# Kernel optimization log

Hardware: AMD Instinct MI355X
Metric: run time of the kernel (lower is better)

## Reference

```python
import jax, jax.numpy as jnp
import numpy as np

N_HEADS = 8
HEAD_D = 64


def setup_inputs() -> dict:
    key = jax.random.key(0)
    ks = jax.random.split(key, 7)
    b, ds, dc = 4, 4096, 256
    ls, lc = 512, 512
    inner = N_HEADS * HEAD_D  # 512
    out_dim = 512
    data = jax.random.normal(ks[0], (b, ds, dc), dtype=jnp.float32)
    latent = jax.random.normal(ks[1], (b, ls, lc), dtype=jnp.float32)
    # torch nn.Linear weights are [out_features, in_features]
    Wq = jax.random.normal(ks[2], (inner, lc), dtype=jnp.float32) * (lc ** -0.5)
    Wk = jax.random.normal(ks[3], (inner, dc), dtype=jnp.float32) * (dc ** -0.5)
    Wv = jax.random.normal(ks[4], (inner, dc), dtype=jnp.float32) * (dc ** -0.5)
    Wo = jax.random.normal(ks[5], (out_dim, inner), dtype=jnp.float32) * (inner ** -0.5)
    bo = jax.random.normal(ks[6], (out_dim,), dtype=jnp.float32) * 0.02
    return {"data": data, "latent": latent, "Wq": Wq, "Wk": Wk, "Wv": Wv, "Wo": Wo, "bo": bo}


def reference(data, latent, Wq, Wk, Wv, Wo, bo):
    b, ds, _ = data.shape
    ls = latent.shape[1]
    scale = HEAD_D ** -0.5
    # projections, split into heads
    Q = (latent @ Wq.T).reshape(b, ls, N_HEADS, HEAD_D)  # [b,ls,h,d]
    K = (data @ Wk.T).reshape(b, ds, N_HEADS, HEAD_D)    # [b,ds,h,d]
    V = (data @ Wv.T).reshape(b, ds, N_HEADS, HEAD_D)
    # logits [b, ds, ls, h]; original broadcasts then sums over head_d -> einsum
    logits = jnp.einsum('blhd,bshd->bslh', Q, K) * scale
    # softmax over key axis (dim 1 = ds), matching attn_logits.softmax(1)
    attn = jax.nn.softmax(logits, axis=1)
    # weighted sum over keys: [b, ls, h, d] -> [b, ls, inner]
    out = jnp.einsum('bshd,bslh->blhd', V, attn).reshape(b, ls, N_HEADS * HEAD_D)
    # output Linear (dropout is identity in eval)
    return out @ Wo.T + bo
```

## Files before the change

kernel.cpp:

```cpp
#include <hip/hip_runtime.h>

typedef __bf16 bf16;
typedef __bf16 bf16x8 __attribute__((ext_vector_type(8)));
typedef float  f32x4  __attribute__((ext_vector_type(4)));

#define LDT 136
#define LDK 72

__device__ __forceinline__ bf16x8 cvt8(float4 a, float4 b) {
    bf16x8 r;
    r[0] = (bf16)a.x; r[1] = (bf16)a.y; r[2] = (bf16)a.z; r[3] = (bf16)a.w;
    r[4] = (bf16)b.x; r[5] = (bf16)b.y; r[6] = (bf16)b.z; r[7] = (bf16)b.w;
    return r;
}

__global__ __launch_bounds__(256) void proj_kvq(
    const float* __restrict__ data, const float* __restrict__ latent,
    const float* __restrict__ Wk, const float* __restrict__ Wv, const float* __restrict__ Wq,
    bf16* __restrict__ K_b, bf16* __restrict__ Vt_b, bf16* __restrict__ Q_b)
{
    __shared__ __align__(16) bf16 arena[128 * LDT];
    bf16* As = arena;
    bf16* Bs = arena + 4096;

    const int bx = blockIdx.x;
    const float* A; const float* Bm; bf16* outb;
    int Kdim, mode, m0, n0;
    if (bx < 512)       { A = data;   Bm = Wk; outb = K_b;  Kdim = 256; mode = 0; m0 = (bx & 127) * 128;         n0 = (bx >> 7) * 128; }
    else if (bx < 1024) { int t = bx - 512;  A = data;   Bm = Wv; outb = Vt_b; Kdim = 256; mode = 1; m0 = (t & 127) * 128; n0 = (t >> 7) * 128; }
    else                { int t = bx - 1024; A = latent; Bm = Wq; outb = Q_b;  Kdim = 512; mode = 2; m0 = (t & 15) * 128;  n0 = (t >> 4) * 128; }

    const int tid = threadIdx.x;
    const int wave = tid >> 6, lane = tid & 63;
    const int wm = wave >> 1, wn = wave & 1;
    const int l15 = lane & 15, quad = lane >> 4;
    const int rowA = tid >> 2;
    const int c8 = (tid & 3) * 8;

    const float* Arow0 = A + (size_t)(m0 + rowA) * Kdim + c8;
    const float* Arow1 = A + (size_t)(m0 + 64 + rowA) * Kdim + c8;
    const float* Brow0 = Bm + (size_t)(n0 + rowA) * Kdim + c8;
    const float* Brow1 = Bm + (size_t)(n0 + 64 + rowA) * Kdim + c8;

    f32x4 acc[4][4] = {};
    float4 a00, a01, a10, a11, b00, b01, b10, b11;

#define LOADP(k) do { \
        a00 = *(const float4*)(Arow0 + (k));  a01 = *(const float4*)(Arow0 + (k) + 4); \
        a10 = *(const float4*)(Arow1 + (k));  a11 = *(const float4*)(Arow1 + (k) + 4); \
        b00 = *(const float4*)(Brow0 + (k));  b01 = *(const float4*)(Brow0 + (k) + 4); \
        b10 = *(const float4*)(Brow1 + (k));  b11 = *(const float4*)(Brow1 + (k) + 4); \
    } while (0)

    LOADP(0);
    for (int k0 = 0; k0 < Kdim; k0 += 32) {
        __syncthreads();
        *(bf16x8*)(As + (size_t)tid * 8)        = cvt8(a00, a01);
        *(bf16x8*)(As + 2048 + (size_t)tid * 8) = cvt8(a10, a11);
        *(bf16x8*)(Bs + (size_t)tid * 8)        = cvt8(b00, b01);
        *(bf16x8*)(Bs + 2048 + (size_t)tid * 8) = cvt8(b10, b11);
        if (k0 + 32 < Kdim) LOADP(k0 + 32);
        __syncthreads();

        bf16x8 af[4], bfr[4];
        #pragma unroll
        for (int mt = 0; mt < 4; mt++)
            af[mt] = *(const bf16x8*)(As + (wm * 64 + mt * 16 + l15) * 32 + quad * 8);
        #pragma unroll
        for (int nt = 0; nt < 4; nt++)
            bfr[nt] = *(const bf16x8*)(Bs + (wn * 64 + nt * 16 + l15) * 32 + quad * 8);
        #pragma unroll
        for (int mt = 0; mt < 4; mt++)
            #pragma unroll
            for (int nt = 0; nt < 4; nt++)
                acc[mt][nt] = __builtin_amdgcn_mfma_f32_16x16x32_bf16(af[mt], bfr[nt], acc[mt][nt], 0, 0, 0);
    }
#undef LOADP

    __syncthreads();
    #pragma unroll
    for (int mt = 0; mt < 4; mt++) {
        #pragma unroll
        for (int nt = 0; nt < 4; nt++) {
            #pragma unroll
            for (int r = 0; r < 4; r++) {
                int ml = wm * 64 + mt * 16 + quad * 4 + r;
                int nl = wn * 64 + nt * 16 + l15;
                bf16 v = (bf16)acc[mt][nt][r];
                if (mode == 1) arena[nl * LDT + ml] = v;
                else           arena[ml * LDT + nl] = v;
            }
        }
    }
    __syncthreads();

    #pragma unroll
    for (int c = 0; c < 8; c++) {
        int idx = c * 256 + tid;
        int row = idx >> 4, col = (idx & 15) * 8;
        bf16x8 vv = *(const bf16x8*)(arena + row * LDT + col);
        if (mode == 0) {
            int m = m0 + row, n = n0 + col;
            *(bf16x8*)(outb + (size_t)((m >> 12) * 8 + (n >> 6)) * 262144 + (m & 4095) * 64 + (n & 63)) = vv;
        } else if (mode == 1) {
            int d = n0 + row, s = m0 + col;
            *(bf16x8*)(outb + (size_t)((s >> 12) * 8 + (d >> 6)) * 262144 + (d & 63) * 4096 + (s & 4095)) = vv;
        } else {
            int m = m0 + row, n = n0 + col;
            *(bf16x8*)(outb + (size_t)((m >> 9) * 8 + (n >> 6)) * 32768 + (m & 511) * 64 + (n & 63)) = vv;
        }
    }
}

__global__ __launch_bounds__(256) void flash_attn(
    const bf16* __restrict__ Q, const bf16* __restrict__ K, const bf16* __restrict__ Vt,
    float* __restrict__ Opart, float* __restrict__ lbuf)
{
    __shared__ bf16 Ks[64 * LDK];
    __shared__ bf16 Vs[64 * LDK];
    __shared__ bf16 Ps[4][16 * LDK];

    const int tid = threadIdx.x;
    const int bx = blockIdx.x;
    const int qp = bx >> 7, bh = (bx >> 2) & 31, ks = bx & 3;
    const int wave = tid >> 6, lane = tid & 63;
    const int l15 = lane & 15, quad = lane >> 4;

    bf16x8 aq[2][2];
    #pragma unroll
    for (int qs = 0; qs < 2; qs++) {
        const bf16* Qb = Q + (size_t)bh * 32768 + (size_t)((qp + qs * 4) * 64 + wave * 16 + l15) * 64;
        aq[qs][0] = *(const bf16x8*)(Qb + quad * 8);
        aq[qs][1] = *(const bf16x8*)(Qb + 32 + quad * 8);
    }
    const bf16* Kb = K + (size_t)bh * 262144;
    const bf16* Vb = Vt + (size_t)bh * 262144;

    f32x4 oacc[2][4] = {};
    float lpart[2][4] = {};
    const float scale = 0.125f;

    const int r0 = tid >> 3, c0 = (tid & 7) * 8;
    const int r1 = (tid + 256) >> 3, c1 = ((tid + 256) & 7) * 8;
    const int kstart = ks * 1024, kend = kstart + 1024;

    uint4 pk0 = *(const uint4*)(Kb + (size_t)(kstart + r0) * 64 + c0);
    uint4 pk1 = *(const uint4*)(Kb + (size_t)(kstart + r1) * 64 + c1);
    uint4 pv0 = *(const uint4*)(Vb + (size_t)r0 * 4096 + kstart + c0);
    uint4 pv1 = *(const uint4*)(Vb + (size_t)r1 * 4096 + kstart + c1);

    for (int key0 = kstart; key0 < kend; key0 += 64) {
        __syncthreads();
        *(uint4*)(Ks + r0 * LDK + c0) = pk0;
        *(uint4*)(Ks + r1 * LDK + c1) = pk1;
        *(uint4*)(Vs + r0 * LDK + c0) = pv0;
        *(uint4*)(Vs + r1 * LDK + c1) = pv1;
        if (key0 + 64 < kend) {
            pk0 = *(const uint4*)(Kb + (size_t)(key0 + 64 + r0) * 64 + c0);
            pk1 = *(const uint4*)(Kb + (size_t)(key0 + 64 + r1) * 64 + c1);
            pv0 = *(const uint4*)(Vb + (size_t)r0 * 4096 + key0 + 64 + c0);
            pv1 = *(const uint4*)(Vb + (size_t)r1 * 4096 + key0 + 64 + c1);
        }
        __syncthreads();

        #pragma unroll
        for (int qs = 0; qs < 2; qs++) {
            float p[4][4];
            #pragma unroll
            for (int nt = 0; nt < 4; nt++) {
                f32x4 z = {};
                #pragma unroll
                for (int kf = 0; kf < 2; kf++) {
                    bf16x8 bk = *(const bf16x8*)(Ks + (nt * 16 + l15) * LDK + kf * 32 + quad * 8);
                    z = __builtin_amdgcn_mfma_f32_16x16x32_bf16(aq[qs][kf], bk, z, 0, 0, 0);
                }
                #pragma unroll
                for (int r = 0; r < 4; r++) {
                    float e = __expf(z[r] * scale);
                    p[r][nt] = e;
                    lpart[qs][r] += e;
                }
            }
            #pragma unroll
            for (int r = 0; r < 4; r++)
                #pragma unroll
                for (int nt = 0; nt < 4; nt++)
                    Ps[wave][(quad * 4 + r) * LDK + nt * 16 + l15] = (bf16)p[r][nt];

            bf16x8 ap[2];
            ap[0] = *(const bf16x8*)(&Ps[wave][l15 * LDK + quad * 8]);
            ap[1] = *(const bf16x8*)(&Ps[wave][l15 * LDK + 32 + quad * 8]);
            #pragma unroll
            for (int dt = 0; dt < 4; dt++) {
                #pragma unroll
                for (int kf = 0; kf < 2; kf++) {
                    bf16x8 bv = *(const bf16x8*)(Vs + (dt * 16 + l15) * LDK + kf * 32 + quad * 8);
                    oacc[qs][dt] = __builtin_amdgcn_mfma_f32_16x16x32_bf16(ap[kf], bv, oacc[qs][dt], 0, 0, 0);
                }
            }
        }
    }

    #pragma unroll
    for (int qs = 0; qs < 2; qs++) {
        #pragma unroll
        for (int r = 0; r < 4; r++) {
            #pragma unroll
            for (int off = 1; off < 16; off <<= 1)
                lpart[qs][r] += __shfl_xor(lpart[qs][r], off, 64);
        }
        const int rowbase = bh * 512 + (qp + qs * 4) * 64 + wave * 16 + quad * 4;
        #pragma unroll
        for (int dt = 0; dt < 4; dt++) {
            #pragma unroll
            for (int r = 0; r < 4; r++)
                Opart[((size_t)ks * 16384 + rowbase + r) * 64 + dt * 16 + l15] = oacc[qs][dt][r];
        }
        if (l15 == 0) {
            #pragma unroll
            for (int r = 0; r < 4; r++)
                lbuf[(size_t)ks * 16384 + rowbase + r] = lpart[qs][r];
        }
    }
}

__global__ __launch_bounds__(256) void gemm_out(
    const float* __restrict__ Opart, const float* __restrict__ lbuf,
    const float* __restrict__ Wo, const float* __restrict__ bo, float* __restrict__ out)
{
    __shared__ bf16 As[64 * 32];
    __shared__ bf16 Bs[64 * 32];
    const int tid = threadIdx.x;
    const int m0 = blockIdx.x * 64, n0 = blockIdx.y * 64;
    const int wave = tid >> 6, lane = tid & 63;
    const int wm = wave >> 1, wn = wave & 1;
    const int l15 = lane & 15, quad = lane >> 4;
    const int rowA = tid >> 2;
    const int c8 = (tid & 3) * 8;
    const int m = m0 + rowA;
    const int mhi = (m >> 9) << 3, mlo = m & 511;

    f32x4 acc[2][2] = {};
    float4 pa[8]; float pl[4]; float4 pb0, pb1;

    auto loadA = [&](int k0) {
        int kc = k0 + c8;
        int arow = (mhi + (kc >> 6)) * 512 + mlo;
        int d0 = kc & 63;
        #pragma unroll
        for (int ks = 0; ks < 4; ks++) {
            pl[ks] = lbuf[(size_t)ks * 16384 + arow];
            pa[2 * ks]     = *(const float4*)(Opart + ((size_t)ks * 16384 + arow) * 64 + d0);
            pa[2 * ks + 1] = *(const float4*)(Opart + ((size_t)ks * 16384 + arow) * 64 + d0 + 4);
        }
    };
    auto loadB = [&](int k0) {
        pb0 = *(const float4*)(Wo + (size_t)(n0 + rowA) * 512 + k0 + c8);
        pb1 = *(const float4*)(Wo + (size_t)(n0 + rowA) * 512 + k0 + c8 + 4);
    };

    loadA(0); loadB(0);

    for (int k0 = 0; k0 < 512; k0 += 32) {
        __syncthreads();
        {
            float L = pl[0] + pl[1] + pl[2] + pl[3];
            float inv = 1.0f / L;
            float4 s0, s1;
            s0.x = pa[0].x + pa[2].x + pa[4].x + pa[6].x;
            s0.y = pa[0].y + pa[2].y + pa[4].y + pa[6].y;
            s0.z = pa[0].z + pa[2].z + pa[4].z + pa[6].z;
            s0.w = pa[0].w + pa[2].w + pa[4].w + pa[6].w;
            s1.x = pa[1].x + pa[3].x + pa[5].x + pa[7].x;
            s1.y = pa[1].y + pa[3].y + pa[5].y + pa[7].y;
            s1.z = pa[1].z + pa[3].z + pa[5].z + pa[7].z;
            s1.w = pa[1].w + pa[3].w + pa[5].w + pa[7].w;
            s0.x *= inv; s0.y *= inv; s0.z *= inv; s0.w *= inv;
            s1.x *= inv; s1.y *= inv; s1.z *= inv; s1.w *= inv;
            *(bf16x8*)(As + (size_t)tid * 8) = cvt8(s0, s1);
            *(bf16x8*)(Bs + (size_t)tid * 8) = cvt8(pb0, pb1);
        }
        if (k0 + 32 < 512) { loadA(k0 + 32); loadB(k0 + 32); }
        __syncthreads();

        bf16x8 af[2], bfr[2];
        #pragma unroll
        for (int mt = 0; mt < 2; mt++)
            af[mt] = *(const bf16x8*)(As + (wm * 32 + mt * 16 + l15) * 32 + quad * 8);
        #pragma unroll
        for (int nt = 0; nt < 2; nt++)
            bfr[nt] = *(const bf16x8*)(Bs + (wn * 32 + nt * 16 + l15) * 32 + quad * 8);
        #pragma unroll
        for (int mt = 0; mt < 2; mt++)
            #pragma unroll
            for (int nt = 0; nt < 2; nt++)
                acc[mt][nt] = __builtin_amdgcn_mfma_f32_16x16x32_bf16(af[mt], bfr[nt], acc[mt][nt], 0, 0, 0);
    }

    #pragma unroll
    for (int mt = 0; mt < 2; mt++) {
        #pragma unroll
        for (int nt = 0; nt < 2; nt++) {
            #pragma unroll
            for (int r = 0; r < 4; r++) {
                int mm = m0 + wm * 32 + mt * 16 + quad * 4 + r;
                int nn = n0 + wn * 32 + nt * 16 + l15;
                out[(size_t)mm * 512 + nn] = acc[mt][nt][r] + bo[nn];
            }
        }
    }
}

extern "C" void kernel_launch(void* const* d_in, const int* in_sizes, int n_in,
                              void* d_out, int out_size, void* d_ws, size_t ws_size,
                              hipStream_t stream) {
    const float* data   = (const float*)d_in[0];
    const float* latent = (const float*)d_in[1];
    const float* Wq = (const float*)d_in[2];
    const float* Wk = (const float*)d_in[3];
    const float* Wv = (const float*)d_in[4];
    const float* Wo = (const float*)d_in[5];
    const float* bo = (const float*)d_in[6];
    float* out = (float*)d_out;

    bf16* ws = (bf16*)d_ws;
    bf16* Q_b    = ws;
    bf16* K_b    = Q_b + 1048576;
    bf16* Vt_b   = K_b + 8388608;
    float* Opart = (float*)(Vt_b + 8388608);
    float* lbuf  = Opart + 4 * 16384 * 64;

    proj_kvq<<<1088, 256, 0, stream>>>(data, latent, Wk, Wv, Wq, K_b, Vt_b, Q_b);
    flash_attn<<<512, 256, 0, stream>>>(Q_b, K_b, Vt_b, Opart, lbuf);
    gemm_out<<<dim3(32, 8), 256, 0, stream>>>(Opart, lbuf, Wo, bo, out);
}
```

Baseline: 164.6 us.

## Halve projection M-tile and split attention keys eight ways for more blocks

The projection GEMM tile shrinks from 128x128 to 64x128, doubling its grid to 2176 blocks and cutting shared memory per block. The flash attention kernel now splits the 4096 keys into 8 chunks of 512 instead of 4 chunks of 1024, doubling its grid to 1024 blocks to fill more CUs. In exchange, the partial-output workspace doubles and the output GEMM must load and reduce 8 partial sums per element. That adds global read traffic and register pressure in gemm_out.

```diff
diff --git a/kernel.cpp b/kernel.cpp
--- a/kernel.cpp
+++ b/kernel.cpp
@@ -5,6 +5,7 @@
 typedef float  f32x4  __attribute__((ext_vector_type(4)));
 
 #define LDT 136
+#define LDV 72
 #define LDK 72
 
 __device__ __forceinline__ bf16x8 cvt8(float4 a, float4 b) {
@@ -19,35 +20,32 @@
     const float* __restrict__ Wk, const float* __restrict__ Wv, const float* __restrict__ Wq,
     bf16* __restrict__ K_b, bf16* __restrict__ Vt_b, bf16* __restrict__ Q_b)
 {
-    __shared__ __align__(16) bf16 arena[128 * LDT];
+    __shared__ __align__(16) bf16 arena[128 * LDV];
     bf16* As = arena;
-    bf16* Bs = arena + 4096;
+    bf16* Bs = arena + 2048;
 
     const int bx = blockIdx.x;
     const float* A; const float* Bm; bf16* outb;
     int Kdim, mode, m0, n0;
-    if (bx < 512)       { A = data;   Bm = Wk; outb = K_b;  Kdim = 256; mode = 0; m0 = (bx & 127) * 128;         n0 = (bx >> 7) * 128; }
-    else if (bx < 1024) { int t = bx - 512;  A = data;   Bm = Wv; outb = Vt_b; Kdim = 256; mode = 1; m0 = (t & 127) * 128; n0 = (t >> 7) * 128; }
-    else                { int t = bx - 1024; A = latent; Bm = Wq; outb = Q_b;  Kdim = 512; mode = 2; m0 = (t & 15) * 128;  n0 = (t >> 4) * 128; }
+    if (bx < 1024)      { A = data;   Bm = Wk; outb = K_b;  Kdim = 256; mode = 0; m0 = (bx & 255) * 64;  n0 = (bx >> 8) * 128; }
+    else if (bx < 2048) { int t = bx - 1024; A = data;   Bm = Wv; outb = Vt_b; Kdim = 256; mode = 1; m0 = (t & 255) * 64; n0 = (t >> 8) * 128; }
+    else                { int t = bx - 2048; A = latent; Bm = Wq; outb = Q_b;  Kdim = 512; mode = 2; m0 = (t & 31) * 64;  n0 = (t >> 5) * 128; }
 
     const int tid = threadIdx.x;
     const int wave = tid >> 6, lane = tid & 63;
-    const int wm = wave >> 1, wn = wave & 1;
     const int l15 = lane & 15, quad = lane >> 4;
-    const int rowA = tid >> 2;
+    const int rowS = tid >> 2;
     const int c8 = (tid & 3) * 8;
 
-    const float* Arow0 = A + (size_t)(m0 + rowA) * Kdim + c8;
-    const float* Arow1 = A + (size_t)(m0 + 64 + rowA) * Kdim + c8;
-    const float* Brow0 = Bm + (size_t)(n0 + rowA) * Kdim + c8;
-    const float* Brow1 = Bm + (size_t)(n0 + 64 + rowA) * Kdim + c8;
-
-    f32x4 acc[4][4] = {};
-    float4 a00, a01, a10, a11, b00, b01, b10, b11;
+    const float* Arow  = A + (size_t)(m0 + rowS) * Kdim + c8;
+    const float* Brow0 = Bm + (size_t)(n0 + rowS) * Kdim + c8;
+    const float* Brow1 = Bm + (size_t)(n0 + 64 + rowS) * Kdim + c8;
+
+    f32x4 acc[4][2] = {};
+    float4 a0, a1, b00, b01, b10, b11;
 
 #define LOADP(k) do { \
-        a00 = *(const float4*)(Arow0 + (k));  a01 = *(const float4*)(Arow0 + (k) + 4); \
-        a10 = *(const float4*)(Arow1 + (k));  a11 = *(const float4*)(Arow1 + (k) + 4); \
+        a0  = *(const float4*)(Arow + (k));   a1  = *(const float4*)(Arow + (k) + 4); \
         b00 = *(const float4*)(Brow0 + (k));  b01 = *(const float4*)(Brow0 + (k) + 4); \
         b10 = *(const float4*)(Brow1 + (k));  b11 = *(const float4*)(Brow1 + (k) + 4); \
     } while (0)
@@ -55,24 +53,23 @@
     LOADP(0);
     for (int k0 = 0; k0 < Kdim; k0 += 32) {
         __syncthreads();
-        *(bf16x8*)(As + (size_t)tid * 8)        = cvt8(a00, a01);
-        *(bf16x8*)(As + 2048 + (size_t)tid * 8) = cvt8(a10, a11);
+        *(bf16x8*)(As + (size_t)tid * 8)        = cvt8(a0, a1);
         *(bf16x8*)(Bs + (size_t)tid * 8)        = cvt8(b00, b01);
         *(bf16x8*)(Bs + 2048 + (size_t)tid * 8) = cvt8(b10, b11);
         if (k0 + 32 < Kdim) LOADP(k0 + 32);
         __syncthreads();
 
-        bf16x8 af[4], bfr[4];
+        bf16x8 af[4], bfr[2];
         #pragma unroll
         for (int mt = 0; mt < 4; mt++)
-            af[mt] = *(const bf16x8*)(As + (wm * 64 + mt * 16 + l15) * 32 + quad * 8);
-        #pragma unroll
-        for (int nt = 0; nt < 4; nt++)
-            bfr[nt] = *(const bf16x8*)(Bs + (wn * 64 + nt * 16 + l15) * 32 + quad * 8);
+            af[mt] = *(const bf16x8*)(As + (mt * 16 + l15) * 32 + quad * 8);
+        #pragma unroll
+        for (int nt = 0; nt < 2; nt++)
+            bfr[nt] = *(const bf16x8*)(Bs + (wave * 32 + nt * 16 + l15) * 32 + quad * 8);
         #pragma unroll
         for (int mt = 0; mt < 4; mt++)
             #pragma unroll
-            for (int nt = 0; nt < 4; nt++)
+            for (int nt = 0; nt < 2; nt++)
                 acc[mt][nt] = __builtin_amdgcn_mfma_f32_16x16x32_bf16(af[mt], bfr[nt], acc[mt][nt], 0, 0, 0);
     }
 #undef LOADP
@@ -81,13 +78,13 @@
     #pragma unroll
     for (int mt = 0; mt < 4; mt++) {
         #pragma unroll
-        for (int nt = 0; nt < 4; nt++) {
+        for (int nt = 0; nt < 2; nt++) {
             #pragma unroll
             for (int r = 0; r < 4; r++) {
-                int ml = wm * 64 + mt * 16 + quad * 4 + r;
-                int nl = wn * 64 + nt * 16 + l15;
+                int ml = mt * 16 + quad * 4 + r;
+                int nl = wave * 32 + nt * 16 + l15;
                 bf16 v = (bf16)acc[mt][nt][r];
-                if (mode == 1) arena[nl * LDT + ml] = v;
+                if (mode == 1) arena[nl * LDV + ml] = v;
                 else           arena[ml * LDT + nl] = v;
             }
         }
@@ -95,19 +92,21 @@
     __syncthreads();
 
     #pragma unroll
-    for (int c = 0; c < 8; c++) {
+    for (int c = 0; c < 4; c++) {
         int idx = c * 256 + tid;
-        int row = idx >> 4, col = (idx & 15) * 8;
-        bf16x8 vv = *(const bf16x8*)(arena + row * LDT + col);
-        if (mode == 0) {
-            int m = m0 + row, n = n0 + col;
-            *(bf16x8*)(outb + (size_t)((m >> 12) * 8 + (n >> 6)) * 262144 + (m & 4095) * 64 + (n & 63)) = vv;
-        } else if (mode == 1) {
+        if (mode == 1) {
+            int row = idx >> 3, col = (idx & 7) * 8;
+            bf16x8 vv = *(const bf16x8*)(arena + row * LDV + col);
             int d = n0 + row, s = m0 + col;
             *(bf16x8*)(outb + (size_t)((s >> 12) * 8 + (d >> 6)) * 262144 + (d & 63) * 4096 + (s & 4095)) = vv;
         } else {
+            int row = idx >> 4, col = (idx & 15) * 8;
+            bf16x8 vv = *(const bf16x8*)(arena + row * LDT + col);
             int m = m0 + row, n = n0 + col;
-            *(bf16x8*)(outb + (size_t)((m >> 9) * 8 + (n >> 6)) * 32768 + (m & 511) * 64 + (n & 63)) = vv;
+            if (mode == 0)
+                *(bf16x8*)(outb + (size_t)((m >> 12) * 8 + (n >> 6)) * 262144 + (m & 4095) * 64 + (n & 63)) = vv;
+            else
+                *(bf16x8*)(outb + (size_t)((m >> 9) * 8 + (n >> 6)) * 32768 + (m & 511) * 64 + (n & 63)) = vv;
         }
     }
 }
@@ -122,7 +121,7 @@
 
     const int tid = threadIdx.x;
     const int bx = blockIdx.x;
-    const int qp = bx >> 7, bh = (bx >> 2) & 31, ks = bx & 3;
+    const int qp = bx >> 8, bh = (bx >> 3) & 31, ks = bx & 7;
     const int wave = tid >> 6, lane = tid & 63;
     const int l15 = lane & 15, quad = lane >> 4;
 
@@ -142,7 +141,7 @@
 
     const int r0 = tid >> 3, c0 = (tid & 7) * 8;
     const int r1 = (tid + 256) >> 3, c1 = ((tid + 256) & 7) * 8;
-    const int kstart = ks * 1024, kend = kstart + 1024;
+    const int kstart = ks * 512, kend = kstart + 512;
 
     uint4 pk0 = *(const uint4*)(Kb + (size_t)(kstart + r0) * 64 + c0);
     uint4 pk1 = *(const uint4*)(Kb + (size_t)(kstart + r1) * 64 + c1);
@@ -241,14 +240,14 @@
     const int mhi = (m >> 9) << 3, mlo = m & 511;
 
     f32x4 acc[2][2] = {};
-    float4 pa[8]; float pl[4]; float4 pb0, pb1;
+    float4 pa[16]; float pl[8]; float4 pb0, pb1;
 
     auto loadA = [&](int k0) {
         int kc = k0 + c8;
         int arow = (mhi + (kc >> 6)) * 512 + mlo;
         int d0 = kc & 63;
         #pragma unroll
-        for (int ks = 0; ks < 4; ks++) {
+        for (int ks = 0; ks < 8; ks++) {
             pl[ks] = lbuf[(size_t)ks * 16384 + arow];
             pa[2 * ks]     = *(const float4*)(Opart + ((size_t)ks * 16384 + arow) * 64 + d0);
             pa[2 * ks + 1] = *(const float4*)(Opart + ((size_t)ks * 16384 + arow) * 64 + d0 + 4);
@@ -264,17 +263,15 @@
     for (int k0 = 0; k0 < 512; k0 += 32) {
         __syncthreads();
         {
-            float L = pl[0] + pl[1] + pl[2] + pl[3];
+            float L = 0.f;
+            float4 s0 = {0.f, 0.f, 0.f, 0.f}, s1 = {0.f, 0.f, 0.f, 0.f};
+            #pragma unroll
+            for (int ks = 0; ks < 8; ks++) {
+                L += pl[ks];
+                s0.x += pa[2 * ks].x; s0.y += pa[2 * ks].y; s0.z += pa[2 * ks].z; s0.w += pa[2 * ks].w;
+                s1.x += pa[2 * ks + 1].x; s1.y += pa[2 * ks + 1].y; s1.z += pa[2 * ks + 1].z; s1.w += pa[2 * ks + 1].w;
+            }
             float inv = 1.0f / L;
-            float4 s0, s1;
-            s0.x = pa[0].x + pa[2].x + pa[4].x + pa[6].x;
-            s0.y = pa[0].y + pa[2].y + pa[4].y + pa[6].y;
-            s0.z = pa[0].z + pa[2].z + pa[4].z + pa[6].z;
-            s0.w = pa[0].w + pa[2].w + pa[4].w + pa[6].w;
-            s1.x = pa[1].x + pa[3].x + pa[5].x + pa[7].x;
-            s1.y = pa[1].y + pa[3].y + pa[5].y + pa[7].y;
-            s1.z = pa[1].z + pa[3].z + pa[5].z + pa[7].z;
-            s1.w = pa[1].w + pa[3].w + pa[5].w + pa[7].w;
             s0.x *= inv; s0.y *= inv; s0.z *= inv; s0.w *= inv;
             s1.x *= inv; s1.y *= inv; s1.z *= inv; s1.w *= inv;
             *(bf16x8*)(As + (size_t)tid * 8) = cvt8(s0, s1);
@@ -328,9 +325,9 @@
     bf16* K_b    = Q_b + 1048576;
     bf16* Vt_b   = K_b + 8388608;
     float* Opart = (float*)(Vt_b + 8388608);
-    float* lbuf  = Opart + 4 * 16384 * 64;
-
-    proj_kvq<<<1088, 256, 0, stream>>>(data, latent, Wk, Wv, Wq, K_b, Vt_b, Q_b);
-    flash_attn<<<512, 256, 0, stream>>>(Q_b, K_b, Vt_b, Opart, lbuf);
+    float* lbuf  = Opart + 8 * 16384 * 64;
+
+    proj_kvq<<<2176, 256, 0, stream>>>(data, latent, Wk, Wv, Wq, K_b, Vt_b, Q_b);
+    flash_attn<<<1024, 256, 0, stream>>>(Q_b, K_b, Vt_b, Opart, lbuf);
     gemm_out<<<dim3(32, 8), 256, 0, stream>>>(Opart, lbuf, Wo, bo, out);
 }
```

Result: faster. 158.6 us (-3.6%).
